# Kernel optimization log

Measured on AMD Instinct MI355X. Metric: run time of the kernel, lower is better.

Reference implementation:

```python
import jax, jax.numpy as jnp
import numpy as np

B, E, F_DIM, D = 32, 16, 64, 512  # batch, extra dim, fea_dim, input_dim
EXP = 4                            # feed-forward expansion
EPS = 1e-5


def _layernorm(x, g, b):
    m = jnp.mean(x, axis=-1, keepdims=True)
    v = jnp.mean(jnp.square(x - m), axis=-1, keepdims=True)
    return (x - m) * jax.lax.rsqrt(v + EPS) * g + b


def setup_inputs() -> dict:
    key = jax.random.key(0)
    ks = jax.random.split(key, 12)
    s = 1.0 / np.sqrt(D)
    inp = {
        "x": jax.random.normal(ks[0], (B, E, F_DIM, D), jnp.float32),
        "ln1_g": jnp.ones((D,), jnp.float32),
        "ln1_b": jnp.zeros((D,), jnp.float32),
        "Wq": jax.random.uniform(ks[1], (D, D), jnp.float32, -s, s),
        "bq": jax.random.uniform(ks[2], (D,), jnp.float32, -s, s),
        "Wk": jax.random.uniform(ks[3], (D, D), jnp.float32, -s, s),
        "bk": jax.random.uniform(ks[4], (D,), jnp.float32, -s, s),
        "Wv": jax.random.uniform(ks[5], (D, D), jnp.float32, -s, s),
        "bv": jax.random.uniform(ks[6], (D,), jnp.float32, -s, s),
        "wn_g": jnp.ones((F_DIM,), jnp.float32),
        "wn_b": jnp.zeros((F_DIM,), jnp.float32),
        "ln2_g": jnp.ones((D,), jnp.float32),
        "ln2_b": jnp.zeros((D,), jnp.float32),
        "W1": jax.random.uniform(ks[7], (D, EXP * D), jnp.float32, -s, s),
        "b1": jax.random.uniform(ks[8], (EXP * D,), jnp.float32, -s, s),
        "W2": jax.random.uniform(ks[9], (EXP * D, D), jnp.float32, -1.0 / np.sqrt(EXP * D), 1.0 / np.sqrt(EXP * D)),
        "b2": jax.random.uniform(ks[10], (D,), jnp.float32, -1.0 / np.sqrt(EXP * D), 1.0 / np.sqrt(EXP * D)),
    }
    return inp


def reference(x, ln1_g, ln1_b, Wq, bq, Wk, bk, Wv, bv, wn_g, wn_b, ln2_g, ln2_b, W1, b1, W2, b2):
    # --- Residual 1: LN -> feature multi-head attention (dropout = identity) ---
    h = _layernorm(x, ln1_g, ln1_b)                       # [B,E,F,D]
    q = h @ Wq + bq
    k = h @ Wk + bk
    v = h @ Wv + bv
    energy = jnp.einsum('beqd,bekd->beqk', q, k)          # [B,E,F,F]
    # LayerNorm over the key axis of the raw scores (the fusion-breaking op)
    energy = _layernorm(energy, wn_g, wn_b)
    att = jax.nn.softmax(energy / jnp.sqrt(jnp.float32(D)), axis=-1)
    attn_out = jnp.einsum('beal,belv->beav', att, v)      # [B,E,F,D]
    x = x + attn_out
    # --- Residual 2: LN -> FFN (Linear -> Linear, no activation) ---
    h2 = _layernorm(x, ln2_g, ln2_b)
    ff = (h2 @ W1 + b1) @ W2 + b2
    return x + ff
```

## Files before the change

### kernel.cpp

```cpp
#include <hip/hip_runtime.h>
#include <hip/hip_bf16.h>


#define D_DIM 512
#define NROWS 32768
#define NBE   512

typedef __attribute__((ext_vector_type(8))) short bf16x8;
typedef __attribute__((ext_vector_type(4))) float f32x4;

typedef const __attribute__((address_space(1))) unsigned g_u32;
typedef __attribute__((address_space(3))) unsigned lds_u32;

__device__ __forceinline__ short f2bf(float f) {
  union { float f; unsigned u; } c; c.f = f;
  unsigned u = c.u;
  unsigned r = (u + 0x7FFFu + ((u >> 16) & 1u)) >> 16;
  return (short)r;
}
__device__ __forceinline__ float bf2f(short s) {
  union { unsigned u; float f; } c; c.u = ((unsigned)(unsigned short)s) << 16;
  return c.f;
}

__global__ __launch_bounds__(256) void wconv_kernel(const float* __restrict__ W,
                                                    short* __restrict__ Wt,
                                                    int K, int N) {
  long idx = (long)blockIdx.x * 256 + threadIdx.x;
  if (idx >= (long)K * N) return;
  int n = (int)(idx / K);
  int k = (int)(idx % K);
  Wt[idx] = f2bf(W[(long)k * N + n]);
}

__global__ __launch_bounds__(256) void ln_kernel(const float* __restrict__ x,
                                                 const float* __restrict__ gam,
                                                 const float* __restrict__ bet,
                                                 short* __restrict__ h) {
  const int t = threadIdx.x;
  const long row = (long)blockIdx.x * 4 + (t >> 6);
  const int lane = t & 63;
  const float* xr = x + row * D_DIM + lane * 8;
  float4 a = *(const float4*)xr;
  float4 b = *(const float4*)(xr + 4);
  float xs[8] = {a.x, a.y, a.z, a.w, b.x, b.y, b.z, b.w};
  float s = 0.f, ss = 0.f;
#pragma unroll
  for (int j = 0; j < 8; ++j) { s += xs[j]; ss += xs[j] * xs[j]; }
#pragma unroll
  for (int m = 1; m < 64; m <<= 1) {
    s  += __shfl_xor(s, m);
    ss += __shfl_xor(ss, m);
  }
  float mean = s * (1.f / D_DIM);
  float var  = ss * (1.f / D_DIM) - mean * mean;
  float rstd = rsqrtf(var + 1e-5f);
  union { short sh[8]; int4 v; } o;
#pragma unroll
  for (int j = 0; j < 8; ++j) {
    int d = lane * 8 + j;
    o.sh[j] = f2bf((xs[j] - mean) * rstd * gam[d] + bet[d]);
  }
  *(int4*)&h[row * D_DIM + lane * 8] = o.v;
}

template <int OUT_BF16, int RESID>
__global__ __launch_bounds__(256) void gemm128(
    const short* __restrict__ A, const short* __restrict__ Bt,
    const float* __restrict__ bias0, const float* __restrict__ bias1,
    const float* __restrict__ bias2,
    void* __restrict__ out0, void* __restrict__ out1, void* __restrict__ out2,
    const float* __restrict__ resid, int K, int nsplit) {
  __shared__ short As[128 * 32];
  __shared__ short Bs[128 * 32];
  const int t = threadIdx.x;
  const int wave = t >> 6, lane = t & 63;
  const int lr = lane & 15, g = lane >> 4;
  const int wr = wave >> 1, wc = wave & 1;
  const int m0 = blockIdx.y * 128, n0 = blockIdx.x * 128;

  const int seg = n0 / nsplit;
  const int ncol0 = n0 - seg * nsplit;
  const float* bias = seg == 0 ? bias0 : (seg == 1 ? bias1 : bias2);
  void* outp = seg == 0 ? out0 : (seg == 1 ? out1 : out2);

  const int crow = lane >> 2;
  const int ccol = (lane & 3) * 8;

  f32x4 acc[4][4];
  const f32x4 vzero = {0.f, 0.f, 0.f, 0.f};
#pragma unroll
  for (int mi = 0; mi < 4; ++mi)
#pragma unroll
    for (int ni = 0; ni < 4; ++ni) acc[mi][ni] = vzero;

  for (int k0 = 0; k0 < K; k0 += 32) {
#pragma unroll
    for (int i = 0; i < 2; ++i) {
      const int c = wave * 2 + i;
      const int row = c * 16 + crow;
      __builtin_amdgcn_global_load_lds(
          (g_u32*)&A[(long)(m0 + row) * K + k0 + ccol],
          (lds_u32*)&As[c * 512], 16, 0, 0);
      __builtin_amdgcn_global_load_lds(
          (g_u32*)&Bt[(long)(n0 + row) * K + k0 + ccol],
          (lds_u32*)&Bs[c * 512], 16, 0, 0);
    }
    __syncthreads();
    bf16x8 af[4], bf[4];
#pragma unroll
    for (int mi = 0; mi < 4; ++mi)
      af[mi] = *(const bf16x8*)&As[(wr * 64 + mi * 16 + lr) * 32 + g * 8];
#pragma unroll
    for (int ni = 0; ni < 4; ++ni)
      bf[ni] = *(const bf16x8*)&Bs[(wc * 64 + ni * 16 + lr) * 32 + g * 8];
#pragma unroll
    for (int mi = 0; mi < 4; ++mi)
#pragma unroll
      for (int ni = 0; ni < 4; ++ni)
        acc[mi][ni] = __builtin_amdgcn_mfma_f32_16x16x32_bf16(af[mi], bf[ni], acc[mi][ni], 0, 0, 0);
    __syncthreads();
  }

#pragma unroll
  for (int ni = 0; ni < 4; ++ni) {
    const int col = ncol0 + wc * 64 + ni * 16 + lr;
    const float bv = bias[col];
#pragma unroll
    for (int mi = 0; mi < 4; ++mi) {
#pragma unroll
      for (int r = 0; r < 4; ++r) {
        const long row = m0 + wr * 64 + mi * 16 + g * 4 + r;
        float val = acc[mi][ni][r] + bv;
        if (RESID) val += resid[row * (long)nsplit + col];
        if (OUT_BF16) ((short*)outp)[row * (long)nsplit + col] = f2bf(val);
        else          ((float*)outp)[row * (long)nsplit + col] = val;
      }
    }
  }
}

__global__ __launch_bounds__(256) void attn_kernel(
    const short* __restrict__ q, const short* __restrict__ k,
    const short* __restrict__ v, const float* __restrict__ x,
    const float* __restrict__ wn_g, const float* __restrict__ wn_b,
    float* __restrict__ x1) {
  __shared__ float att_s[64][68];
  const int t = threadIdx.x;
  const int wave = t >> 6, lane = t & 63;
  const int lr = lane & 15, g = lane >> 4;
  const long base = (long)blockIdx.x * 64;
  const long qoff = base * D_DIM;

  const f32x4 vzero = {0.f, 0.f, 0.f, 0.f};
  f32x4 acc[4];
#pragma unroll
  for (int nt = 0; nt < 4; ++nt) acc[nt] = vzero;

  for (int ks = 0; ks < 16; ++ks) {
    const int kc = ks * 32 + g * 8;
    bf16x8 afr = *(const bf16x8*)&q[qoff + (long)(wave * 16 + lr) * D_DIM + kc];
#pragma unroll
    for (int nt = 0; nt < 4; ++nt) {
      bf16x8 bfr = *(const bf16x8*)&k[qoff + (long)(nt * 16 + lr) * D_DIM + kc];
      acc[nt] = __builtin_amdgcn_mfma_f32_16x16x32_bf16(afr, bfr, acc[nt], 0, 0, 0);
    }
  }

  const float scale = 0.044194173824159216f;
#pragma unroll
  for (int r = 0; r < 4; ++r) {
    float s = 0.f, ss = 0.f;
#pragma unroll
    for (int nt = 0; nt < 4; ++nt) { float e = acc[nt][r]; s += e; ss += e * e; }
#pragma unroll
    for (int m = 1; m < 16; m <<= 1) { s += __shfl_xor(s, m); ss += __shfl_xor(ss, m); }
    float mean = s * (1.f / 64);
    float var  = ss * (1.f / 64) - mean * mean;
    float rstd = rsqrtf(var + 1e-5f);
    float e[4]; float mx = -1e30f;
#pragma unroll
    for (int nt = 0; nt < 4; ++nt) {
      int col = nt * 16 + lr;
      e[nt] = ((acc[nt][r] - mean) * rstd * wn_g[col] + wn_b[col]) * scale;
      mx = fmaxf(mx, e[nt]);
    }
#pragma unroll
    for (int m = 1; m < 16; m <<= 1) mx = fmaxf(mx, __shfl_xor(mx, m));
    float se = 0.f;
#pragma unroll
    for (int nt = 0; nt < 4; ++nt) { e[nt] = expf(e[nt] - mx); se += e[nt]; }
#pragma unroll
    for (int m = 1; m < 16; m <<= 1) se += __shfl_xor(se, m);
    float inv = 1.f / se;
#pragma unroll
    for (int nt = 0; nt < 4; ++nt)
      att_s[wave * 16 + 4 * g + r][nt * 16 + lr] = e[nt] * inv;
  }
  __syncthreads();

  const int d0 = lane * 8;
  float accp[16][8];
#pragma unroll
  for (int qi = 0; qi < 16; ++qi)
#pragma unroll
    for (int j = 0; j < 8; ++j) accp[qi][j] = 0.f;

  for (int kk0 = 0; kk0 < 64; kk0 += 4) {
    float vf[4][8];
#pragma unroll
    for (int kc = 0; kc < 4; ++kc) {
      bf16x8 vv = *(const bf16x8*)&v[qoff + (long)(kk0 + kc) * D_DIM + d0];
#pragma unroll
      for (int j = 0; j < 8; ++j) vf[kc][j] = bf2f(vv[j]);
    }
#pragma unroll
    for (int qi = 0; qi < 16; ++qi) {
      float4 a4 = *(const float4*)&att_s[wave * 16 + qi][kk0];
#pragma unroll
      for (int j = 0; j < 8; ++j) {
        accp[qi][j] += a4.x * vf[0][j];
        accp[qi][j] += a4.y * vf[1][j];
        accp[qi][j] += a4.z * vf[2][j];
        accp[qi][j] += a4.w * vf[3][j];
      }
    }
  }
#pragma unroll
  for (int qi = 0; qi < 16; ++qi) {
    long row = base + wave * 16 + qi;
    const float* xr = x + row * D_DIM + d0;
    float* po = x1 + row * D_DIM + d0;
    float4 x0 = *(const float4*)xr;
    float4 xb = *(const float4*)(xr + 4);
    float4 o0, o1;
    o0.x = x0.x + accp[qi][0]; o0.y = x0.y + accp[qi][1];
    o0.z = x0.z + accp[qi][2]; o0.w = x0.w + accp[qi][3];
    o1.x = xb.x + accp[qi][4]; o1.y = xb.y + accp[qi][5];
    o1.z = xb.z + accp[qi][6]; o1.w = xb.w + accp[qi][7];
    *(float4*)po = o0;
    *(float4*)(po + 4) = o1;
  }
}

extern "C" void kernel_launch(void* const* d_in, const int* in_sizes, int n_in,
                              void* d_out, int out_size, void* d_ws, size_t ws_size,
                              hipStream_t stream) {
  (void)in_sizes; (void)n_in; (void)out_size; (void)ws_size;
  const float* x     = (const float*)d_in[0];
  const float* ln1_g = (const float*)d_in[1];
  const float* ln1_b = (const float*)d_in[2];
  const float* Wq    = (const float*)d_in[3];
  const float* bq    = (const float*)d_in[4];
  const float* Wk    = (const float*)d_in[5];
  const float* bk    = (const float*)d_in[6];
  const float* Wv    = (const float*)d_in[7];
  const float* bv    = (const float*)d_in[8];
  const float* wn_g  = (const float*)d_in[9];
  const float* wn_b  = (const float*)d_in[10];
  const float* ln2_g = (const float*)d_in[11];
  const float* ln2_b = (const float*)d_in[12];
  const float* W1    = (const float*)d_in[13];
  const float* b1    = (const float*)d_in[14];
  const float* W2    = (const float*)d_in[15];
  const float* b2    = (const float*)d_in[16];
  float* out = (float*)d_out;

  char* ws = (char*)d_ws;
  short* h   = (short*)(ws);
  short* qb  = (short*)(ws + (size_t)32  * 1024 * 1024);
  short* kb  = (short*)(ws + (size_t)64  * 1024 * 1024);
  short* vb  = (short*)(ws + (size_t)96  * 1024 * 1024);
  short* ff1 = (short*)(ws + (size_t)32  * 1024 * 1024);
  short* Wqt = (short*)(ws + (size_t)160 * 1024 * 1024);
  short* Wkt = Wqt + 512 * 512;
  short* Wvt = Wkt + 512 * 512;
  short* W1t = Wvt + 512 * 512;
  short* W2t = W1t + 512 * 2048;

  wconv_kernel<<<(512 * 512)  / 256, 256, 0, stream>>>(Wq, Wqt, 512, 512);
  wconv_kernel<<<(512 * 512)  / 256, 256, 0, stream>>>(Wk, Wkt, 512, 512);
  wconv_kernel<<<(512 * 512)  / 256, 256, 0, stream>>>(Wv, Wvt, 512, 512);
  wconv_kernel<<<(512 * 2048) / 256, 256, 0, stream>>>(W1, W1t, 512, 2048);
  wconv_kernel<<<(2048 * 512) / 256, 256, 0, stream>>>(W2, W2t, 2048, 512);

  ln_kernel<<<NROWS / 4, 256, 0, stream>>>(x, ln1_g, ln1_b, h);

  dim3 gqkv(1536 / 128, NROWS / 128);
  gemm128<1, 0><<<gqkv, 256, 0, stream>>>(h, Wqt, bq, bk, bv,
                                          qb, kb, vb, nullptr, 512, 512);

  attn_kernel<<<NBE, 256, 0, stream>>>(qb, kb, vb, x, wn_g, wn_b, out);

  ln_kernel<<<NROWS / 4, 256, 0, stream>>>(out, ln2_g, ln2_b, h);

  dim3 gff1(2048 / 128, NROWS / 128);
  gemm128<1, 0><<<gff1, 256, 0, stream>>>(h, W1t, b1, b1, b1,
                                          ff1, ff1, ff1, nullptr, 512, 2048);

  dim3 gff2(512 / 128, NROWS / 128);
  gemm128<0, 1><<<gff2, 256, 0, stream>>>(ff1, W2t, b2, b2, b2,
                                          out, out, out, out, 2048, 512);
}
```

Before: 606.9 us.

## Fuse LN2 into attention epilogue, tile weight transpose, remap GEMM workgroup order

The second LayerNorm is folded into the attention kernel's epilogue. Each wave already holds full 512-wide rows of the residual output, so it reduces mean and variance with shuffles and writes the bf16 normalized activations directly. This removes a separate kernel launch and a full fp32 re-read of the residual. The weight conversion kernel now transposes through a shared-memory tile so reads and writes are coalesced. The GEMM also remaps workgroup IDs across 8 groups, likely to spread tiles over XCDs for better cache locality. One risk is that variance is computed as E[x^2]-mean^2, which is less stable than the two-pass form.

```diff
diff --git a/kernel.cpp b/kernel.cpp
--- a/kernel.cpp
+++ b/kernel.cpp
@@ -23,14 +23,23 @@
   return c.f;
 }
 
-__global__ __launch_bounds__(256) void wconv_kernel(const float* __restrict__ W,
-                                                    short* __restrict__ Wt,
-                                                    int K, int N) {
-  long idx = (long)blockIdx.x * 256 + threadIdx.x;
-  if (idx >= (long)K * N) return;
-  int n = (int)(idx / K);
-  int k = (int)(idx % K);
-  Wt[idx] = f2bf(W[(long)k * N + n]);
+__global__ __launch_bounds__(256) void wconvT(const float* __restrict__ W,
+                                              short* __restrict__ Wt,
+                                              int K, int N) {
+  __shared__ float tile[32][33];
+  const int t = threadIdx.x;
+  const int r  = t >> 3;
+  const int c4 = (t & 7) * 4;
+  const long k0 = (long)blockIdx.y * 32;
+  const long n0 = (long)blockIdx.x * 32;
+  float4 v = *(const float4*)&W[(k0 + r) * N + n0 + c4];
+  tile[r][c4 + 0] = v.x; tile[r][c4 + 1] = v.y;
+  tile[r][c4 + 2] = v.z; tile[r][c4 + 3] = v.w;
+  __syncthreads();
+  union { short sh[4]; int2 v; } o;
+#pragma unroll
+  for (int j = 0; j < 4; ++j) o.sh[j] = f2bf(tile[c4 + j][r]);
+  *(int2*)&Wt[(n0 + r) * K + k0 + c4] = o.v;
 }
 
 __global__ __launch_bounds__(256) void ln_kernel(const float* __restrict__ x,
@@ -77,7 +86,13 @@
   const int wave = t >> 6, lane = t & 63;
   const int lr = lane & 15, g = lane >> 4;
   const int wr = wave >> 1, wc = wave & 1;
-  const int m0 = blockIdx.y * 128, n0 = blockIdx.x * 128;
+
+  const int gx = gridDim.x;
+  const int nwg = gx * gridDim.y;
+  const int hid = blockIdx.y * gx + blockIdx.x;
+  const int lid = (hid & 7) * (nwg >> 3) + (hid >> 3);
+  const int m0 = (lid / gx) * 128;
+  const int n0 = (lid % gx) * 128;
 
   const int seg = n0 / nsplit;
   const int ncol0 = n0 - seg * nsplit;
@@ -144,7 +159,8 @@
     const short* __restrict__ q, const short* __restrict__ k,
     const short* __restrict__ v, const float* __restrict__ x,
     const float* __restrict__ wn_g, const float* __restrict__ wn_b,
-    float* __restrict__ x1) {
+    const float* __restrict__ ln2_g, const float* __restrict__ ln2_b,
+    float* __restrict__ x1, short* __restrict__ h2) {
   __shared__ float att_s[64][68];
   const int t = threadIdx.x;
   const int wave = t >> 6, lane = t & 63;
@@ -226,20 +242,37 @@
       }
     }
   }
+
+  float g2v[8], b2v[8];
+#pragma unroll
+  for (int j = 0; j < 8; ++j) { g2v[j] = ln2_g[d0 + j]; b2v[j] = ln2_b[d0 + j]; }
+
 #pragma unroll
   for (int qi = 0; qi < 16; ++qi) {
-    long row = base + wave * 16 + qi;
+    const long row = base + wave * 16 + qi;
     const float* xr = x + row * D_DIM + d0;
-    float* po = x1 + row * D_DIM + d0;
     float4 x0 = *(const float4*)xr;
     float4 xb = *(const float4*)(xr + 4);
-    float4 o0, o1;
-    o0.x = x0.x + accp[qi][0]; o0.y = x0.y + accp[qi][1];
-    o0.z = x0.z + accp[qi][2]; o0.w = x0.w + accp[qi][3];
-    o1.x = xb.x + accp[qi][4]; o1.y = xb.y + accp[qi][5];
-    o1.z = xb.z + accp[qi][6]; o1.w = xb.w + accp[qi][7];
-    *(float4*)po = o0;
-    *(float4*)(po + 4) = o1;
+    accp[qi][0] += x0.x; accp[qi][1] += x0.y;
+    accp[qi][2] += x0.z; accp[qi][3] += x0.w;
+    accp[qi][4] += xb.x; accp[qi][5] += xb.y;
+    accp[qi][6] += xb.z; accp[qi][7] += xb.w;
+    float* po = x1 + row * D_DIM + d0;
+    *(float4*)po       = make_float4(accp[qi][0], accp[qi][1], accp[qi][2], accp[qi][3]);
+    *(float4*)(po + 4) = make_float4(accp[qi][4], accp[qi][5], accp[qi][6], accp[qi][7]);
+    float s = 0.f, ss = 0.f;
+#pragma unroll
+    for (int j = 0; j < 8; ++j) { s += accp[qi][j]; ss += accp[qi][j] * accp[qi][j]; }
+#pragma unroll
+    for (int m = 1; m < 64; m <<= 1) { s += __shfl_xor(s, m); ss += __shfl_xor(ss, m); }
+    float mean = s * (1.f / D_DIM);
+    float var  = ss * (1.f / D_DIM) - mean * mean;
+    float rstd = rsqrtf(var + 1e-5f);
+    union { short sh[8]; int4 v; } o;
+#pragma unroll
+    for (int j = 0; j < 8; ++j)
+      o.sh[j] = f2bf((accp[qi][j] - mean) * rstd * g2v[j] + b2v[j]);
+    *(int4*)&h2[row * D_DIM + d0] = o.v;
   }
 }
 
@@ -278,11 +311,11 @@
   short* W1t = Wvt + 512 * 512;
   short* W2t = W1t + 512 * 2048;
 
-  wconv_kernel<<<(512 * 512)  / 256, 256, 0, stream>>>(Wq, Wqt, 512, 512);
-  wconv_kernel<<<(512 * 512)  / 256, 256, 0, stream>>>(Wk, Wkt, 512, 512);
-  wconv_kernel<<<(512 * 512)  / 256, 256, 0, stream>>>(Wv, Wvt, 512, 512);
-  wconv_kernel<<<(512 * 2048) / 256, 256, 0, stream>>>(W1, W1t, 512, 2048);
-  wconv_kernel<<<(2048 * 512) / 256, 256, 0, stream>>>(W2, W2t, 2048, 512);
+  wconvT<<<dim3(512 / 32, 512 / 32),  256, 0, stream>>>(Wq, Wqt, 512, 512);
+  wconvT<<<dim3(512 / 32, 512 / 32),  256, 0, stream>>>(Wk, Wkt, 512, 512);
+  wconvT<<<dim3(512 / 32, 512 / 32),  256, 0, stream>>>(Wv, Wvt, 512, 512);
+  wconvT<<<dim3(2048 / 32, 512 / 32), 256, 0, stream>>>(W1, W1t, 512, 2048);
+  wconvT<<<dim3(512 / 32, 2048 / 32), 256, 0, stream>>>(W2, W2t, 2048, 512);
 
   ln_kernel<<<NROWS / 4, 256, 0, stream>>>(x, ln1_g, ln1_b, h);
 
@@ -290,9 +323,8 @@
   gemm128<1, 0><<<gqkv, 256, 0, stream>>>(h, Wqt, bq, bk, bv,
                                           qb, kb, vb, nullptr, 512, 512);
 
-  attn_kernel<<<NBE, 256, 0, stream>>>(qb, kb, vb, x, wn_g, wn_b, out);
-
-  ln_kernel<<<NROWS / 4, 256, 0, stream>>>(out, ln2_g, ln2_b, h);
+  attn_kernel<<<NBE, 256, 0, stream>>>(qb, kb, vb, x, wn_g, wn_b,
+                                       ln2_g, ln2_b, out, h);
 
   dim3 gff1(2048 / 128, NROWS / 128);
   gemm128<1, 0><<<gff1, 256, 0, stream>>>(h, W1t, b1, b1, b1,
```

After: 571.7 us. 5.8% less time.
